# Kernel optimization log

Measured on AMD Instinct MI355X. Metric: run time of the kernel, lower is better.

Reference implementation:

```python
import jax, jax.numpy as jnp
import numpy as np

N_A = 100000; N_B = 100000; E = 1600000
H = 128; OUT = 16; G = 256; D_A = 64; D_B = 32


def setup_inputs() -> dict:
    key = jax.random.key(0)
    ks = jax.random.split(key, 24)
    f32 = jnp.float32
    def w(k, shape, fan_in):
        return jax.random.normal(k, shape, dtype=f32) / np.sqrt(fan_in)
    inp = {
        'x_a': jax.random.normal(ks[0], (N_A, D_A), dtype=f32),
        'x_b': jax.random.normal(ks[1], (N_B, D_B), dtype=f32),
        'ei_ab': jax.random.randint(ks[2], (2, E), 0, N_A),  # row0: src in a, row1: dst in b
        'ei_ba': jax.random.randint(ks[3], (2, E), 0, N_B),
        'ei_aa': jax.random.randint(ks[4], (2, E), 0, N_A),
        'batch_a': jnp.sort(jax.random.randint(ks[5], (N_A,), 0, G)),
        'batch_b': jnp.sort(jax.random.randint(ks[6], (N_B,), 0, G)),
        # node-type input embeddings
        'Wemb_a': w(ks[7], (D_A, H), D_A), 'bemb_a': jnp.zeros((H,), f32),
        'Wemb_b': w(ks[8], (D_B, H), D_B), 'bemb_b': jnp.zeros((H,), f32),
        # SAGEConv params per relation: lin_l (with bias) on aggregated, lin_r (no bias) on root
        'Wl_ab': w(ks[9], (H, H), H), 'bl_ab': jnp.zeros((H,), f32), 'Wr_ab': w(ks[10], (H, H), H),
        'Wl_ba': w(ks[11], (H, H), H), 'bl_ba': jnp.zeros((H,), f32), 'Wr_ba': w(ks[12], (H, H), H),
        'Wl_aa': w(ks[13], (H, H), H), 'bl_aa': jnp.zeros((H,), f32), 'Wr_aa': w(ks[14], (H, H), H),
        # output head
        'Wout': w(ks[15], (H, OUT), H), 'bout': jnp.zeros((OUT,), f32),
    }
    return inp


def _sage(x_src, x_dst, ei, Wl, bl, Wr, n_dst):
    # mean aggregation of source features over incoming edges, then transform + root
    msg = x_src[ei[0]]                                        # [E, H] gather
    s = jax.ops.segment_sum(msg, ei[1], num_segments=n_dst)   # [n_dst, H]
    cnt = jax.ops.segment_sum(jnp.ones((ei.shape[1], 1), x_src.dtype), ei[1], num_segments=n_dst)
    agg = s / jnp.maximum(cnt, 1.0)
    return agg @ Wl + bl + x_dst @ Wr


def _mean_pool(x, batch, num_graphs):
    s = jax.ops.segment_sum(x, batch, num_segments=num_graphs)
    cnt = jax.ops.segment_sum(jnp.ones((x.shape[0], 1), x.dtype), batch, num_segments=num_graphs)
    return s / jnp.maximum(cnt, 1.0)


def reference(x_a, x_b, ei_ab, ei_ba, ei_aa, batch_a, batch_b,
              Wemb_a, bemb_a, Wemb_b, bemb_b,
              Wl_ab, bl_ab, Wr_ab, Wl_ba, bl_ba, Wr_ba, Wl_aa, bl_aa, Wr_aa,
              Wout, bout):
    # per-type input projection
    h_a = x_a @ Wemb_a + bemb_a            # [N_A, H]
    h_b = x_b @ Wemb_b + bemb_b            # [N_B, H]
    # HeteroConv: one SAGEConv per relation, mean over relations per dst type
    m_b = _sage(h_a, h_b, ei_ab, Wl_ab, bl_ab, Wr_ab, N_B)          # dst 'b': 1 relation
    m_a1 = _sage(h_b, h_a, ei_ba, Wl_ba, bl_ba, Wr_ba, N_A)
    m_a2 = _sage(h_a, h_a, ei_aa, Wl_aa, bl_aa, Wr_aa, N_A)
    h_a2 = 0.5 * (m_a1 + m_a2)                                      # dst 'a': mean of 2 relations
    h_b2 = m_b
    # ReLU + per-type global mean pool + mean over node types
    p_a = _mean_pool(jax.nn.relu(h_a2), batch_a, G)                 # [G, H]
    p_b = _mean_pool(jax.nn.relu(h_b2), batch_b, G)
    x = 0.5 * (p_a + p_b)
    return x @ Wout + bout                                          # [G, OUT]
```

## Files before the change

### kernel.cpp

```cpp
#include <hip/hip_runtime.h>

#define NA 100000
#define NB 100000
#define NEDGE 1600000
#define HD 128
#define OUTD 16
#define NG 256
#define DA 64
#define DB 32
#define PG 8

#define BIN_SHIFT 9
#define BIN_W 512
#define NBINS_R 196
#define NBINS 588
#define PADBIN 10240
#define EPB 8192
#define ECHUNKS 196

typedef unsigned int uint_t;
typedef unsigned short ushort_t;
typedef unsigned char uchar_t;
typedef __bf16 bf16_t;
typedef bf16_t bf16x8 __attribute__((ext_vector_type(8)));
typedef float f32x4 __attribute__((ext_vector_type(4)));
typedef float f32x2 __attribute__((ext_vector_type(2)));

__device__ __forceinline__ float bflo(uint_t u) {
    union { uint_t i; float f; } c; c.i = u << 16; return c.f;
}
__device__ __forceinline__ float bfhi(uint_t u) {
    union { uint_t i; float f; } c; c.i = u & 0xffff0000u; return c.f;
}
__device__ __forceinline__ uint_t f2bf(float f) {
    union { float f; uint_t i; } c; c.f = f;
    uint_t r = c.i + 0x7FFFu + ((c.i >> 16) & 1u);
    return r >> 16;
}
__device__ __forceinline__ uint_t pack2bf(float lo, float hi) {
    return f2bf(lo) | (f2bf(hi) << 16);
}

__global__ void __launch_bounds__(256)
prep_misc_kernel(const float* __restrict__ Wl_ab, const float* __restrict__ Wr_ab,
                 const float* __restrict__ Wl_ba, const float* __restrict__ Wl_aa,
                 const float* __restrict__ Wr_ba, const float* __restrict__ Wr_aa,
                 const float* __restrict__ Wemb_a, const float* __restrict__ Wemb_b,
                 ushort_t* __restrict__ wt_fb, ushort_t* __restrict__ wt_pa,
                 ushort_t* __restrict__ wt_ea, ushort_t* __restrict__ wt_eb,
                 const float* __restrict__ bl_ba, const float* __restrict__ bl_aa,
                 float* __restrict__ bias_pa,
                 const int* __restrict__ batch_a, const int* __restrict__ batch_b,
                 float* __restrict__ ga, float* __restrict__ gb)
{
    const int bx = blockIdx.x;
    if (bx >= 40) {
        __align__(16) ushort_t tmp[8];
        if (bx <= 43) {
            const int id = (bx - 40) * 256 + threadIdx.x;
            const int nn = id >> 3, ck = id & 7;
#pragma unroll
            for (int j = 0; j < 8; ++j) tmp[j] = (ushort_t)f2bf(Wemb_a[(ck * 8 + j) * HD + nn]);
            const int swz = ck ^ (nn & 7);
            *reinterpret_cast<uint4*>(wt_ea + nn * 64 + swz * 8) = *reinterpret_cast<const uint4*>(tmp);
            return;
        }
        if (bx <= 45) {
            const int id = (bx - 44) * 256 + threadIdx.x;
            const int nn = id >> 2, ck = id & 3;
#pragma unroll
            for (int j = 0; j < 8; ++j) tmp[j] = (ushort_t)f2bf(Wemb_b[(ck * 8 + j) * HD + nn]);
            const int swz = ck ^ (nn & 3);
            *reinterpret_cast<uint4*>(wt_eb + nn * 32 + swz * 8) = *reinterpret_cast<const uint4*>(tmp);
            return;
        }
        if (bx == 46) {
            if (threadIdx.x < HD) bias_pa[threadIdx.x] = bl_ba[threadIdx.x] + bl_aa[threadIdx.x];
            return;
        }
        const int g = threadIdx.x;
        const int* batch = (bx == 48) ? batch_b : batch_a;
        float* outp = (bx == 48) ? gb : ga;
        const int n = NA;
        int lo0 = 0, hi0 = n;
        while (lo0 < hi0) { const int mid = (lo0 + hi0) >> 1; if (batch[mid] < g) lo0 = mid + 1; else hi0 = mid; }
        int lo1 = 0, hi1 = n;
        while (lo1 < hi1) { const int mid = (lo1 + hi1) >> 1; if (batch[mid] < g + 1) lo1 = mid + 1; else hi1 = mid; }
        outp[g] = (float)(lo1 - lo0);
        return;
    }
    const int m = bx >> 3;
    const int id = (bx & 7) * 256 + threadIdx.x;
    const int nn = id >> 4, ck = id & 15;
    const float* src = (m == 0) ? Wl_ab : (m == 1) ? Wr_ab : (m == 2) ? Wl_ba
                     : (m == 3) ? Wl_aa : Wr_ba;
    __align__(16) ushort_t tmp[8];
#pragma unroll
    for (int j = 0; j < 8; ++j) {
        const int k = ck * 8 + j;
        float v = src[k * HD + nn];
        if (m == 4) v += Wr_aa[k * HD + nn];
        tmp[j] = (ushort_t)f2bf(v);
    }
    const int cks = ck ^ (nn & 7);
    const int half = nn >> 6, nl = nn & 63;
    ushort_t* dst = (m < 2) ? (wt_fb + half * 16384 + m * 8192)
                            : (wt_pa + half * 24576 + (m - 2) * 8192);
    *reinterpret_cast<uint4*>(dst + nl * HD + cks * 8) = *reinterpret_cast<const uint4*>(tmp);
}

template<int K>
__global__ void __launch_bounds__(256)
emb_mfma(const float* __restrict__ x, const ushort_t* __restrict__ wt,
         const float* __restrict__ bias, ushort_t* __restrict__ h, int n)
{
    constexpr int NCK = K / 8;
    constexpr int KST = K / 32;
    __shared__ ushort_t wlds[HD * K];
    __shared__ float bias_lds[HD];
    for (int i = threadIdx.x * 8; i < HD * K; i += 2048)
        *reinterpret_cast<uint4*>(wlds + i) = *reinterpret_cast<const uint4*>(wt + i);
    if (threadIdx.x < HD) bias_lds[threadIdx.x] = bias[threadIdx.x];
    __syncthreads();
    const int l = threadIdx.x & 63, w = threadIdx.x >> 6;
    const int lo = l & 15, hi = l >> 4;
    const int row_base = blockIdx.x * 128 + w * 32;

    f32x4 acc[2][8];
    const f32x4 zero = {0.f, 0.f, 0.f, 0.f};
#pragma unroll
    for (int mi = 0; mi < 2; ++mi)
#pragma unroll
        for (int ni = 0; ni < 8; ++ni) acc[mi][ni] = zero;

    bf16x8 a[2][KST];
#pragma unroll
    for (int mi = 0; mi < 2; ++mi) {
        int r = row_base + mi * 16 + lo;
        r = min(r, n - 1);
        const float* xr = x + (size_t)r * K + hi * 8;
#pragma unroll
        for (int kk = 0; kk < KST; ++kk) {
            const float4 f0 = *reinterpret_cast<const float4*>(xr + kk * 32);
            const float4 f1 = *reinterpret_cast<const float4*>(xr + kk * 32 + 4);
            __align__(16) ushort_t us[8];
            us[0] = (ushort_t)f2bf(f0.x); us[1] = (ushort_t)f2bf(f0.y);
            us[2] = (ushort_t)f2bf(f0.z); us[3] = (ushort_t)f2bf(f0.w);
            us[4] = (ushort_t)f2bf(f1.x); us[5] = (ushort_t)f2bf(f1.y);
            us[6] = (ushort_t)f2bf(f1.z); us[7] = (ushort_t)f2bf(f1.w);
            a[mi][kk] = *reinterpret_cast<const bf16x8*>(us);
        }
    }
#pragma unroll
    for (int kk = 0; kk < KST; ++kk) {
#pragma unroll
        for (int ni = 0; ni < 8; ++ni) {
            const int nn = ni * 16 + lo;
            const int ck = (kk * 4 + hi) ^ (nn & (NCK - 1));
            const bf16x8 b = *reinterpret_cast<const bf16x8*>(wlds + nn * K + ck * 8);
            acc[0][ni] = __builtin_amdgcn_mfma_f32_16x16x32_bf16(a[0][kk], b, acc[0][ni], 0, 0, 0);
            acc[1][ni] = __builtin_amdgcn_mfma_f32_16x16x32_bf16(a[1][kk], b, acc[1][ni], 0, 0, 0);
        }
    }
#pragma unroll
    for (int mi = 0; mi < 2; ++mi) {
#pragma unroll
        for (int ni = 0; ni < 8; ++ni) {
            const int col = ni * 16 + lo;
            const float bv = bias_lds[col];
            const f32x4 v = acc[mi][ni];
#pragma unroll
            for (int r = 0; r < 4; ++r) {
                const int row = row_base + mi * 16 + hi * 4 + r;
                if (row < n) h[(size_t)row * HD + col] = (ushort_t)f2bf(v[r] + bv);
            }
        }
    }
}

__global__ void __launch_bounds__(256)
conv8_kernel(const ushort_t* __restrict__ h, uchar_t* __restrict__ h8, long n8)
{
    for (long i = (long)blockIdx.x * 256 + threadIdx.x; i < n8; i += (long)gridDim.x * 256) {
        const uint4 v = *reinterpret_cast<const uint4*>(h + i * 8);
        uint_t lo = (uint_t)__builtin_amdgcn_cvt_pk_fp8_f32(bflo(v.x), bfhi(v.x), 0, false);
        lo = (uint_t)__builtin_amdgcn_cvt_pk_fp8_f32(bflo(v.y), bfhi(v.y), lo, true);
        uint_t hi = (uint_t)__builtin_amdgcn_cvt_pk_fp8_f32(bflo(v.z), bfhi(v.z), 0, false);
        hi = (uint_t)__builtin_amdgcn_cvt_pk_fp8_f32(bflo(v.w), bfhi(v.w), hi, true);
        uint2 o; o.x = lo; o.y = hi;
        *reinterpret_cast<uint2*>(h8 + i * 8) = o;
    }
}

__global__ void __launch_bounds__(256)
part3_kernel(const int* __restrict__ ei_ab, const int* __restrict__ ei_ba,
             const int* __restrict__ ei_aa, int* __restrict__ bincnt,
             uint_t* __restrict__ binned)
{
    __shared__ uint_t sorted[EPB];
    __shared__ int lh[NBINS_R];
    __shared__ int lbase[NBINS_R];
    __shared__ int gbase[NBINS_R];
    __shared__ int lcur[NBINS_R];
    __shared__ int sc[256];
    const int r = blockIdx.y;
    const int* ei = (r == 0) ? ei_ab : (r == 1) ? ei_ba : ei_aa;
    const int t = threadIdx.x;
    for (int i = t; i < NBINS_R; i += 256) lh[i] = 0;
    __syncthreads();
    const int e0 = blockIdx.x * EPB;
    const int e1 = min(e0 + EPB, NEDGE);
    for (int e = e0 + t; e < e1; e += 256)
        atomicAdd(&lh[ei[NEDGE + e] >> BIN_SHIFT], 1);
    __syncthreads();
    {
        const int v = (t < NBINS_R) ? lh[t] : 0;
        sc[t] = v; __syncthreads();
        for (int d = 1; d < 256; d <<= 1) {
            const int x = (t >= d) ? sc[t - d] : 0;
            __syncthreads();
            sc[t] += x;
            __syncthreads();
        }
        if (t < NBINS_R) {
            const int ex = sc[t] - v;
            lbase[t] = ex; lcur[t] = ex;
            gbase[t] = v ? atomicAdd(&bincnt[r * NBINS_R + t], v) : 0;
        }
    }
    __syncthreads();
    for (int e = e0 + t; e < e1; e += 256) {
        const int dst = ei[NEDGE + e];
        const int src = ei[e];
        const int bin = dst >> BIN_SHIFT;
        const int pos = atomicAdd(&lcur[bin], 1);
        sorted[pos] = ((uint_t)(dst & (BIN_W - 1)) << 17) | (uint_t)src;
    }
    __syncthreads();
    const int wid = t >> 6, lane = t & 63;
    for (int b = wid; b < NBINS_R; b += 4) {
        const int cnt = lh[b], lb = lbase[b];
        uint_t* dst = binned + (size_t)(r * NBINS_R + b) * PADBIN + gbase[b];
        for (int k = lane; k < cnt; k += 64) dst[k] = sorted[lb + k];
    }
}

__global__ void __launch_bounds__(256)
binfill3_kernel(const uint_t* __restrict__ binned, const int* __restrict__ bincnt,
                int* __restrict__ off3, int* __restrict__ cnt3, int* __restrict__ csr3)
{
    __shared__ int hist[BIN_W];
    __shared__ int A[BIN_W];
    __shared__ int cursor[BIN_W];
    const int b = blockIdx.x;
    const int r = blockIdx.y;
    const int g = r * NBINS_R + b;
    const int start = g * PADBIN;
    const int end = start + bincnt[g];
    const int t = threadIdx.x;
    const int i0 = t, i1 = t + 256;
    hist[i0] = 0; hist[i1] = 0;
    __syncthreads();
    for (int j = start + t; j < end; j += 256)
        atomicAdd(&hist[binned[j] >> 17], 1);
    __syncthreads();
    A[i0] = hist[i0]; A[i1] = hist[i1];
    __syncthreads();
    for (int d = 1; d < BIN_W; d <<= 1) {
        const int x0 = (i0 >= d) ? A[i0 - d] : 0;
        const int x1 = (i1 >= d) ? A[i1 - d] : 0;
        __syncthreads();
        A[i0] += x0; A[i1] += x1;
        __syncthreads();
    }
    const int node0 = b * BIN_W;
#pragma unroll
    for (int q = 0; q < 2; ++q) {
        const int i = t + q * 256;
        const int ex = start + A[i] - hist[i];
        cursor[i] = ex;
        const int node = node0 + i;
        if (node < NA) { off3[r * NA + node] = ex; cnt3[r * NA + node] = hist[i]; }
    }
    __syncthreads();
    for (int j = start + t; j < end; j += 256) {
        const uint_t p = binned[j];
        const int pos = atomicAdd(&cursor[p >> 17], 1);
        csr3[pos] = (int)(p & 0x1FFFFu);
    }
}

__global__ void __launch_bounds__(256)
gather3_kernel(const uchar_t* __restrict__ h8_a, const uchar_t* __restrict__ h8_b,
               const int* __restrict__ csr3, const int* __restrict__ off3,
               const int* __restrict__ cnt3,
               ushort_t* __restrict__ s_ab, ushort_t* __restrict__ s_ba,
               ushort_t* __restrict__ s_aa)
{
    const int r = blockIdx.y;
    const uchar_t* hsrc = (r == 1) ? h8_b : h8_a;
    ushort_t* s = (r == 0) ? s_ab : (r == 1) ? s_ba : s_aa;
    const int* off = off3 + r * NA;
    const int* cnt = cnt3 + r * NA;
    const int wid = threadIdx.x >> 6, lane = threadIdx.x & 63;
    const int hl = lane & 31;
    const int nw = gridDim.x * 4;
    for (int node = blockIdx.x * 4 + wid; node < NA; node += nw) {
        const int o0 = off[node], deg = cnt[node];
        const int o1 = o0 + deg;
        float ax0 = 0.f, ax1 = 0.f, ax2 = 0.f, ax3 = 0.f;
        int j = o0;
        for (; j + 8 <= o1; j += 8) {
            const int s0 = csr3[j],     s1 = csr3[j + 1], s2 = csr3[j + 2], s3 = csr3[j + 3];
            const int s4 = csr3[j + 4], s5 = csr3[j + 5], s6 = csr3[j + 6], s7 = csr3[j + 7];
            const int sA = (lane & 32) ? s1 : s0;
            const int sB = (lane & 32) ? s3 : s2;
            const int sC = (lane & 32) ? s5 : s4;
            const int sD = (lane & 32) ? s7 : s6;
            const uint_t vA = *reinterpret_cast<const uint_t*>(hsrc + (size_t)sA * HD + hl * 4);
            const uint_t vB = *reinterpret_cast<const uint_t*>(hsrc + (size_t)sB * HD + hl * 4);
            const uint_t vC = *reinterpret_cast<const uint_t*>(hsrc + (size_t)sC * HD + hl * 4);
            const uint_t vD = *reinterpret_cast<const uint_t*>(hsrc + (size_t)sD * HD + hl * 4);
            const f32x2 a0 = __builtin_amdgcn_cvt_pk_f32_fp8(vA, false), a1 = __builtin_amdgcn_cvt_pk_f32_fp8(vA, true);
            const f32x2 b0 = __builtin_amdgcn_cvt_pk_f32_fp8(vB, false), b1 = __builtin_amdgcn_cvt_pk_f32_fp8(vB, true);
            const f32x2 c0 = __builtin_amdgcn_cvt_pk_f32_fp8(vC, false), c1 = __builtin_amdgcn_cvt_pk_f32_fp8(vC, true);
            const f32x2 d0 = __builtin_amdgcn_cvt_pk_f32_fp8(vD, false), d1 = __builtin_amdgcn_cvt_pk_f32_fp8(vD, true);
            ax0 += (a0[0] + b0[0]) + (c0[0] + d0[0]);
            ax1 += (a0[1] + b0[1]) + (c0[1] + d0[1]);
            ax2 += (a1[0] + b1[0]) + (c1[0] + d1[0]);
            ax3 += (a1[1] + b1[1]) + (c1[1] + d1[1]);
        }
        for (; j + 2 <= o1; j += 2) {
            const int s0 = csr3[j], s1 = csr3[j + 1];
            const int sA = (lane & 32) ? s1 : s0;
            const uint_t vA = *reinterpret_cast<const uint_t*>(hsrc + (size_t)sA * HD + hl * 4);
            const f32x2 a0 = __builtin_amdgcn_cvt_pk_f32_fp8(vA, false), a1 = __builtin_amdgcn_cvt_pk_f32_fp8(vA, true);
            ax0 += a0[0]; ax1 += a0[1]; ax2 += a1[0]; ax3 += a1[1];
        }
        if (j < o1) {
            const int s0 = csr3[j];
            const uint_t vA = *reinterpret_cast<const uint_t*>(hsrc + (size_t)s0 * HD + hl * 4);
            if (!(lane & 32)) {
                const f32x2 a0 = __builtin_amdgcn_cvt_pk_f32_fp8(vA, false), a1 = __builtin_amdgcn_cvt_pk_f32_fp8(vA, true);
                ax0 += a0[0]; ax1 += a0[1]; ax2 += a1[0]; ax3 += a1[1];
            }
        }
        ax0 += __shfl_xor(ax0, 32); ax1 += __shfl_xor(ax1, 32);
        ax2 += __shfl_xor(ax2, 32); ax3 += __shfl_xor(ax3, 32);
        if (!(lane & 32)) {
            const float inv = 1.0f / fmaxf((float)deg, 1.0f);
            uint2 wv;
            wv.x = pack2bf(ax0 * inv, ax1 * inv);
            wv.y = pack2bf(ax2 * inv, ax3 * inv);
            *reinterpret_cast<uint2*>(s + (size_t)node * HD + hl * 4) = wv;
        }
    }
}

template<int NSRC, int SCALE_HALF>
__device__ __forceinline__ void
mfma_body(const ushort_t* __restrict__ x0, const ushort_t* __restrict__ x1,
          const ushort_t* __restrict__ x2,
          const ushort_t* __restrict__ wts, const float* __restrict__ bias,
          const int* __restrict__ batch, float* __restrict__ outp, int n,
          char* smem)
{
    ushort_t* wlds   = (ushort_t*)smem;
    float* bias_lds  = (float*)(smem + NSRC * 16384);
    float* poolbuf   = bias_lds + HD;

    const int l  = threadIdx.x & 63, w = threadIdx.x >> 6;
    const int lo = l & 15, hi = l >> 4;
    const int row_base = blockIdx.x * 128 + w * 32;

    bf16x8 a[NSRC][2][4];
#pragma unroll
    for (int s = 0; s < NSRC; ++s) {
        const ushort_t* xs = (s == 0) ? x0 : (s == 1) ? x1 : x2;
#pragma unroll
        for (int mi = 0; mi < 2; ++mi) {
            int r = row_base + mi * 16 + lo;
            r = min(r, n - 1);
            const ushort_t* xr = xs + (size_t)r * HD + hi * 8;
#pragma unroll
            for (int kk = 0; kk < 4; ++kk)
                a[s][mi][kk] = *reinterpret_cast<const bf16x8*>(xr + kk * 32);
        }
    }
    if (threadIdx.x < HD) bias_lds[threadIdx.x] = bias[threadIdx.x];
    const int gmin = batch[blockIdx.x * 128];

    for (int half = 0; half < 2; ++half) {
        __syncthreads();
        const ushort_t* wsrc = wts + (size_t)half * NSRC * 8192;
        for (int i = threadIdx.x * 8; i < NSRC * 8192; i += 256 * 8)
            *reinterpret_cast<uint4*>(wlds + i) = *reinterpret_cast<const uint4*>(wsrc + i);
        for (int i = threadIdx.x; i < PG * 64; i += 256) poolbuf[i] = 0.f;
        __syncthreads();

        f32x4 acc[2][4];
        const f32x4 zero = {0.f, 0.f, 0.f, 0.f};
#pragma unroll
        for (int mi = 0; mi < 2; ++mi)
#pragma unroll
            for (int ni = 0; ni < 4; ++ni) acc[mi][ni] = zero;

#pragma unroll
        for (int s = 0; s < NSRC; ++s) {
            const ushort_t* wb = wlds + s * 8192;
#pragma unroll
            for (int kk = 0; kk < 4; ++kk) {
#pragma unroll
                for (int ni = 0; ni < 4; ++ni) {
                    const int nn = ni * 16 + lo;
                    const int ck = (kk * 4 + hi) ^ (nn & 7);
                    const bf16x8 b = *reinterpret_cast<const bf16x8*>(wb + nn * HD + ck * 8);
                    acc[0][ni] = __builtin_amdgcn_mfma_f32_16x16x32_bf16(a[s][0][kk], b, acc[0][ni], 0, 0, 0);
                    acc[1][ni] = __builtin_amdgcn_mfma_f32_16x16x32_bf16(a[s][1][kk], b, acc[1][ni], 0, 0, 0);
                }
            }
        }

#pragma unroll
        for (int mi = 0; mi < 2; ++mi) {
#pragma unroll
            for (int ni = 0; ni < 4; ++ni) {
                const int col_l = ni * 16 + lo;
                const int col = half * 64 + col_l;
                const float bv = bias_lds[col];
                const f32x4 v = acc[mi][ni];
#pragma unroll
                for (int r = 0; r < 4; ++r) {
                    const int row = row_base + mi * 16 + hi * 4 + r;
                    if (row < n) {
                        float val = v[r] + bv;
                        if (SCALE_HALF) val *= 0.5f;
                        val = fmaxf(val, 0.f);
                        const int g = batch[row];
                        const unsigned slot = (unsigned)(g - gmin);
                        if (slot < PG) atomicAdd(&poolbuf[slot * 64 + col_l], val);
                        else unsafeAtomicAdd(outp + (size_t)g * HD + col, val);
                    }
                }
            }
        }
        __syncthreads();
        for (int i = threadIdx.x; i < PG * 64; i += 256) {
            const float v = poolbuf[i];
            if (v != 0.f) {
                const int g = gmin + (i >> 6);
                if (g < NG) unsafeAtomicAdd(outp + (size_t)g * HD + half * 64 + (i & 63), v);
            }
        }
    }
}

__global__ void __launch_bounds__(256)
mfma_both(const ushort_t* __restrict__ s_ab, const ushort_t* __restrict__ h_b,
          const ushort_t* __restrict__ wt_fb, const float* __restrict__ bl_ab,
          const int* __restrict__ batch_b, float* __restrict__ pool_b,
          const ushort_t* __restrict__ s_ba, const ushort_t* __restrict__ s_aa,
          const ushort_t* __restrict__ h_a,
          const ushort_t* __restrict__ wt_pa, const float* __restrict__ bias_pa,
          const int* __restrict__ batch_a, float* __restrict__ pool_a)
{
    extern __shared__ char smem[];
    if (blockIdx.y == 0)
        mfma_body<2, 0>(s_ab, h_b, nullptr, wt_fb, bl_ab, batch_b, pool_b, NB, smem);
    else
        mfma_body<3, 1>(s_ba, s_aa, h_a, wt_pa, bias_pa, batch_a, pool_a, NA, smem);
}

__global__ void final_kernel(const float* __restrict__ pa, const float* __restrict__ pb,
                             const float* __restrict__ ga, const float* __restrict__ gb,
                             const float* __restrict__ Wout, const float* __restrict__ bout,
                             float* __restrict__ out)
{
    const int g = blockIdx.x;
    const int lane = threadIdx.x;
    const float inva = 1.0f / fmaxf(ga[g], 1.0f);
    const float invb = 1.0f / fmaxf(gb[g], 1.0f);
    if (lane < OUTD) {
        float acc = bout[lane];
        for (int k = 0; k < HD; ++k) {
            const float x = 0.5f * (pa[g * HD + k] * inva + pb[g * HD + k] * invb);
            acc = fmaf(x, Wout[k * OUTD + lane], acc);
        }
        out[g * OUTD + lane] = acc;
    }
}

extern "C" void kernel_launch(void* const* d_in, const int* in_sizes, int n_in,
                              void* d_out, int out_size, void* d_ws, size_t ws_size,
                              hipStream_t stream)
{
    const float* x_a     = (const float*)d_in[0];
    const float* x_b     = (const float*)d_in[1];
    const int*   ei_ab   = (const int*)d_in[2];
    const int*   ei_ba   = (const int*)d_in[3];
    const int*   ei_aa   = (const int*)d_in[4];
    const int*   batch_a = (const int*)d_in[5];
    const int*   batch_b = (const int*)d_in[6];
    const float* Wemb_a  = (const float*)d_in[7];
    const float* bemb_a  = (const float*)d_in[8];
    const float* Wemb_b  = (const float*)d_in[9];
    const float* bemb_b  = (const float*)d_in[10];
    const float* Wl_ab   = (const float*)d_in[11];
    const float* bl_ab   = (const float*)d_in[12];
    const float* Wr_ab   = (const float*)d_in[13];
    const float* Wl_ba   = (const float*)d_in[14];
    const float* bl_ba   = (const float*)d_in[15];
    const float* Wr_ba   = (const float*)d_in[16];
    const float* Wl_aa   = (const float*)d_in[17];
    const float* bl_aa   = (const float*)d_in[18];
    const float* Wr_aa   = (const float*)d_in[19];
    const float* Wout    = (const float*)d_in[20];
    const float* bout    = (const float*)d_in[21];
    float* out = (float*)d_out;

    char* p = (char*)d_ws;
    ushort_t* h_a  = (ushort_t*)p; p += (size_t)NA * HD * 2;
    ushort_t* h_b  = (ushort_t*)p; p += (size_t)NB * HD * 2;
    ushort_t* s_ab = (ushort_t*)p; p += (size_t)NB * HD * 2;
    ushort_t* s_ba = (ushort_t*)p; p += (size_t)NA * HD * 2;
    ushort_t* s_aa = (ushort_t*)p; p += (size_t)NA * HD * 2;
    uchar_t* h8_a  = (uchar_t*)p;  p += (size_t)NA * HD;
    uchar_t* h8_b  = (uchar_t*)p;  p += (size_t)NB * HD;
    int* csr3   = (int*)p;  p += (size_t)NBINS * PADBIN * 4;
    uint_t* binned = (uint_t*)p; p += (size_t)NBINS * PADBIN * 4;
    int* off3   = (int*)p;  p += (size_t)3 * NA * 4;
    int* cnt3   = (int*)p;  p += (size_t)3 * NA * 4;
    int* bincnt = (int*)p;  p += (NBINS + 4) * 4;
    float* pool_a = (float*)p; p += (size_t)NG * HD * 4;
    float* pool_b = (float*)p; p += (size_t)NG * HD * 4;
    float* gcnt_a = (float*)p; p += NG * 4;
    float* gcnt_b = (float*)p; p += NG * 4;
    ushort_t* wt_fb = (ushort_t*)p; p += 2 * 16384 * 2;
    ushort_t* wt_pa = (ushort_t*)p; p += 3 * 16384 * 2;
    ushort_t* wt_ea = (ushort_t*)p; p += 64 * HD * 2;
    ushort_t* wt_eb = (ushort_t*)p; p += 32 * HD * 2;
    float* bias_pa  = (float*)p;    p += HD * 4;

    const int GT = (NA + 127) / 128;

    hipMemsetAsync(pool_a, 0, (size_t)2 * NG * HD * 4, stream);
    hipMemsetAsync(bincnt, 0, (size_t)NBINS * 4, stream);

    prep_misc_kernel<<<49, 256, 0, stream>>>(Wl_ab, Wr_ab, Wl_ba, Wl_aa, Wr_ba, Wr_aa,
                                             Wemb_a, Wemb_b, wt_fb, wt_pa, wt_ea, wt_eb,
                                             bl_ba, bl_aa, bias_pa,
                                             batch_a, batch_b, gcnt_a, gcnt_b);

    emb_mfma<DA><<<GT, 256, 0, stream>>>(x_a, wt_ea, bemb_a, h_a, NA);
    emb_mfma<DB><<<GT, 256, 0, stream>>>(x_b, wt_eb, bemb_b, h_b, NB);
    conv8_kernel<<<2048, 256, 0, stream>>>(h_a, h8_a, (long)(NA + NB) * HD / 8);

    part3_kernel<<<dim3(ECHUNKS, 3), 256, 0, stream>>>(ei_ab, ei_ba, ei_aa, bincnt, binned);
    binfill3_kernel<<<dim3(NBINS_R, 3), 256, 0, stream>>>(binned, bincnt, off3, cnt3, csr3);

    gather3_kernel<<<dim3(2048, 3), 256, 0, stream>>>(h8_a, h8_b, csr3, off3, cnt3, s_ab, s_ba, s_aa);

    const int lds_m = 3 * 16384 + 512 + PG * 64 * 4;
    hipFuncSetAttribute((const void*)mfma_both, hipFuncAttributeMaxDynamicSharedMemorySize, lds_m);
    mfma_both<<<dim3(GT, 2), 256, lds_m, stream>>>(s_ab, h_b, wt_fb, bl_ab, batch_b, pool_b,
                                                   s_ba, s_aa, h_a, wt_pa, bias_pa, batch_a, pool_a);

    final_kernel<<<NG, 64, 0, stream>>>(pool_a, pool_b, gcnt_a, gcnt_b, Wout, bout, out);
}
```

Measured before the change: 462.0 us.

## Pre-swizzle weights into MFMA fragment order and load B operands directly from global

Result: slower. 552.1 us (+19.5%).

```diff
diff --git a/kernel.cpp b/kernel.cpp
--- a/kernel.cpp
+++ b/kernel.cpp
@@ -54,24 +54,26 @@
                  float* __restrict__ ga, float* __restrict__ gb)
 {
     const int bx = blockIdx.x;
+    __align__(16) ushort_t tmp[8];
     if (bx >= 40) {
-        __align__(16) ushort_t tmp[8];
         if (bx <= 43) {
             const int id = (bx - 40) * 256 + threadIdx.x;
-            const int nn = id >> 3, ck = id & 7;
-#pragma unroll
-            for (int j = 0; j < 8; ++j) tmp[j] = (ushort_t)f2bf(Wemb_a[(ck * 8 + j) * HD + nn]);
-            const int swz = ck ^ (nn & 7);
-            *reinterpret_cast<uint4*>(wt_ea + nn * 64 + swz * 8) = *reinterpret_cast<const uint4*>(tmp);
+            const int kk = id >> 9, ni = (id >> 6) & 7, l = id & 63;
+            const int col = ni * 16 + (l & 15);
+            const int k0 = kk * 32 + (l >> 4) * 8;
+#pragma unroll
+            for (int j = 0; j < 8; ++j) tmp[j] = (ushort_t)f2bf(Wemb_a[(k0 + j) * HD + col]);
+            *reinterpret_cast<uint4*>(wt_ea + (size_t)id * 8) = *reinterpret_cast<const uint4*>(tmp);
             return;
         }
         if (bx <= 45) {
             const int id = (bx - 44) * 256 + threadIdx.x;
-            const int nn = id >> 2, ck = id & 3;
-#pragma unroll
-            for (int j = 0; j < 8; ++j) tmp[j] = (ushort_t)f2bf(Wemb_b[(ck * 8 + j) * HD + nn]);
-            const int swz = ck ^ (nn & 3);
-            *reinterpret_cast<uint4*>(wt_eb + nn * 32 + swz * 8) = *reinterpret_cast<const uint4*>(tmp);
+            const int ni = id >> 6, l = id & 63;
+            const int col = ni * 16 + (l & 15);
+            const int k0 = (l >> 4) * 8;
+#pragma unroll
+            for (int j = 0; j < 8; ++j) tmp[j] = (ushort_t)f2bf(Wemb_b[(k0 + j) * HD + col]);
+            *reinterpret_cast<uint4*>(wt_eb + (size_t)id * 8) = *reinterpret_cast<const uint4*>(tmp);
             return;
         }
         if (bx == 46) {
@@ -91,37 +93,27 @@
     }
     const int m = bx >> 3;
     const int id = (bx & 7) * 256 + threadIdx.x;
-    const int nn = id >> 4, ck = id & 15;
+    const int kk = id >> 9, ni = (id >> 6) & 7, l = id & 63;
+    const int col = ni * 16 + (l & 15);
+    const int k0 = kk * 32 + (l >> 4) * 8;
     const float* src = (m == 0) ? Wl_ab : (m == 1) ? Wr_ab : (m == 2) ? Wl_ba
                      : (m == 3) ? Wl_aa : Wr_ba;
-    __align__(16) ushort_t tmp[8];
 #pragma unroll
     for (int j = 0; j < 8; ++j) {
-        const int k = ck * 8 + j;
-        float v = src[k * HD + nn];
-        if (m == 4) v += Wr_aa[k * HD + nn];
+        float v = src[(k0 + j) * HD + col];
+        if (m == 4) v += Wr_aa[(k0 + j) * HD + col];
         tmp[j] = (ushort_t)f2bf(v);
     }
-    const int cks = ck ^ (nn & 7);
-    const int half = nn >> 6, nl = nn & 63;
-    ushort_t* dst = (m < 2) ? (wt_fb + half * 16384 + m * 8192)
-                            : (wt_pa + half * 24576 + (m - 2) * 8192);
-    *reinterpret_cast<uint4*>(dst + nl * HD + cks * 8) = *reinterpret_cast<const uint4*>(tmp);
+    ushort_t* dst = (m < 2) ? (wt_fb + (size_t)m * 16384) : (wt_pa + (size_t)(m - 2) * 16384);
+    *reinterpret_cast<uint4*>(dst + (size_t)id * 8) = *reinterpret_cast<const uint4*>(tmp);
 }
 
 template<int K>
 __global__ void __launch_bounds__(256)
-emb_mfma(const float* __restrict__ x, const ushort_t* __restrict__ wt,
+emb_mfma(const float* __restrict__ x, const ushort_t* __restrict__ wtf,
          const float* __restrict__ bias, ushort_t* __restrict__ h, int n)
 {
-    constexpr int NCK = K / 8;
     constexpr int KST = K / 32;
-    __shared__ ushort_t wlds[HD * K];
-    __shared__ float bias_lds[HD];
-    for (int i = threadIdx.x * 8; i < HD * K; i += 2048)
-        *reinterpret_cast<uint4*>(wlds + i) = *reinterpret_cast<const uint4*>(wt + i);
-    if (threadIdx.x < HD) bias_lds[threadIdx.x] = bias[threadIdx.x];
-    __syncthreads();
     const int l = threadIdx.x & 63, w = threadIdx.x >> 6;
     const int lo = l & 15, hi = l >> 4;
     const int row_base = blockIdx.x * 128 + w * 32;
@@ -155,19 +147,17 @@
     for (int kk = 0; kk < KST; ++kk) {
 #pragma unroll
         for (int ni = 0; ni < 8; ++ni) {
-            const int nn = ni * 16 + lo;
-            const int ck = (kk * 4 + hi) ^ (nn & (NCK - 1));
-            const bf16x8 b = *reinterpret_cast<const bf16x8*>(wlds + nn * K + ck * 8);
+            const bf16x8 b = *reinterpret_cast<const bf16x8*>(wtf + ((size_t)(kk * 8 + ni) * 64 + l) * 8);
             acc[0][ni] = __builtin_amdgcn_mfma_f32_16x16x32_bf16(a[0][kk], b, acc[0][ni], 0, 0, 0);
             acc[1][ni] = __builtin_amdgcn_mfma_f32_16x16x32_bf16(a[1][kk], b, acc[1][ni], 0, 0, 0);
         }
     }
 #pragma unroll
-    for (int mi = 0; mi < 2; ++mi) {
-#pragma unroll
-        for (int ni = 0; ni < 8; ++ni) {
-            const int col = ni * 16 + lo;
-            const float bv = bias_lds[col];
+    for (int ni = 0; ni < 8; ++ni) {
+        const int col = ni * 16 + lo;
+        const float bv = bias[col];
+#pragma unroll
+        for (int mi = 0; mi < 2; ++mi) {
             const f32x4 v = acc[mi][ni];
 #pragma unroll
             for (int r = 0; r < 4; ++r) {
@@ -358,25 +348,31 @@
 }
 
 template<int NSRC, int SCALE_HALF>
-__device__ __forceinline__ void
-mfma_body(const ushort_t* __restrict__ x0, const ushort_t* __restrict__ x1,
+__global__ void __launch_bounds__(256)
+mfma_task(const ushort_t* __restrict__ x0, const ushort_t* __restrict__ x1,
           const ushort_t* __restrict__ x2,
-          const ushort_t* __restrict__ wts, const float* __restrict__ bias,
-          const int* __restrict__ batch, float* __restrict__ outp, int n,
-          char* smem)
-{
-    ushort_t* wlds   = (ushort_t*)smem;
-    float* bias_lds  = (float*)(smem + NSRC * 16384);
-    float* poolbuf   = bias_lds + HD;
+          const ushort_t* __restrict__ wtf, const float* __restrict__ bias,
+          const int* __restrict__ batch, float* __restrict__ outp, int n)
+{
+    __shared__ float poolbuf[PG * HD];
+    for (int i = threadIdx.x; i < PG * HD; i += 256) poolbuf[i] = 0.f;
+    __syncthreads();
 
     const int l  = threadIdx.x & 63, w = threadIdx.x >> 6;
     const int lo = l & 15, hi = l >> 4;
     const int row_base = blockIdx.x * 128 + w * 32;
 
-    bf16x8 a[NSRC][2][4];
+    f32x4 acc[2][8];
+    const f32x4 zero = {0.f, 0.f, 0.f, 0.f};
+#pragma unroll
+    for (int mi = 0; mi < 2; ++mi)
+#pragma unroll
+        for (int ni = 0; ni < 8; ++ni) acc[mi][ni] = zero;
+
 #pragma unroll
     for (int s = 0; s < NSRC; ++s) {
         const ushort_t* xs = (s == 0) ? x0 : (s == 1) ? x1 : x2;
+        bf16x8 a[2][4];
 #pragma unroll
         for (int mi = 0; mi < 2; ++mi) {
             int r = row_base + mi * 16 + lo;
@@ -384,91 +380,59 @@
             const ushort_t* xr = xs + (size_t)r * HD + hi * 8;
 #pragma unroll
             for (int kk = 0; kk < 4; ++kk)
-                a[s][mi][kk] = *reinterpret_cast<const bf16x8*>(xr + kk * 32);
-        }
-    }
-    if (threadIdx.x < HD) bias_lds[threadIdx.x] = bias[threadIdx.x];
+                a[mi][kk] = *reinterpret_cast<const bf16x8*>(xr + kk * 32);
+        }
+        const ushort_t* wm = wtf + (size_t)s * 16384;
+#pragma unroll
+        for (int kk = 0; kk < 4; ++kk) {
+#pragma unroll
+            for (int ni = 0; ni < 8; ++ni) {
+                const bf16x8 b = *reinterpret_cast<const bf16x8*>(wm + ((size_t)(kk * 8 + ni) * 64 + l) * 8);
+                acc[0][ni] = __builtin_amdgcn_mfma_f32_16x16x32_bf16(a[0][kk], b, acc[0][ni], 0, 0, 0);
+                acc[1][ni] = __builtin_amdgcn_mfma_f32_16x16x32_bf16(a[1][kk], b, acc[1][ni], 0, 0, 0);
+            }
+        }
+    }
+
     const int gmin = batch[blockIdx.x * 128];
-
-    for (int half = 0; half < 2; ++half) {
-        __syncthreads();
-        const ushort_t* wsrc = wts + (size_t)half * NSRC * 8192;
-        for (int i = threadIdx.x * 8; i < NSRC * 8192; i += 256 * 8)
-            *reinterpret_cast<uint4*>(wlds + i) = *reinterpret_cast<const uint4*>(wsrc + i);
-        for (int i = threadIdx.x; i < PG * 64; i += 256) poolbuf[i] = 0.f;
-        __syncthreads();
-
-        f32x4 acc[2][4];
-        const f32x4 zero = {0.f, 0.f, 0.f, 0.f};
-#pragma unroll
-        for (int mi = 0; mi < 2; ++mi)
-#pragma unroll
-            for (int ni = 0; ni < 4; ++ni) acc[mi][ni] = zero;
-
-#pragma unroll
-        for (int s = 0; s < NSRC; ++s) {
-            const ushort_t* wb = wlds + s * 8192;
-#pragma unroll
-            for (int kk = 0; kk < 4; ++kk) {
-#pragma unroll
-                for (int ni = 0; ni < 4; ++ni) {
-                    const int nn = ni * 16 + lo;
-                    const int ck = (kk * 4 + hi) ^ (nn & 7);
-                    const bf16x8 b = *reinterpret_cast<const bf16x8*>(wb + nn * HD + ck * 8);
-                    acc[0][ni] = __builtin_amdgcn_mfma_f32_16x16x32_bf16(a[s][0][kk], b, acc[0][ni], 0, 0, 0);
-                    acc[1][ni] = __builtin_amdgcn_mfma_f32_16x16x32_bf16(a[s][1][kk], b, acc[1][ni], 0, 0, 0);
+    int gg[2][4];
+#pragma unroll
+    for (int mi = 0; mi < 2; ++mi)
+#pragma unroll
+        for (int r = 0; r < 4; ++r) {
+            const int row = row_base + mi * 16 + hi * 4 + r;
+            gg[mi][r] = (row < n) ? batch[row] : -1;
+        }
+
+#pragma unroll
+    for (int ni = 0; ni < 8; ++ni) {
+        const int col = ni * 16 + lo;
+        const float bv = bias[col];
+#pragma unroll
+        for (int mi = 0; mi < 2; ++mi) {
+            const f32x4 v = acc[mi][ni];
+#pragma unroll
+            for (int r = 0; r < 4; ++r) {
+                const int g = gg[mi][r];
+                if (g >= 0) {
+                    float val = v[r] + bv;
+                    if (SCALE_HALF) val *= 0.5f;
+                    val = fmaxf(val, 0.f);
+                    const unsigned slot = (unsigned)(g - gmin);
+                    if (slot < PG) atomicAdd(&poolbuf[slot * HD + col], val);
+                    else unsafeAtomicAdd(outp + (size_t)g * HD + col, val);
                 }
             }
         }
-
-#pragma unroll
-        for (int mi = 0; mi < 2; ++mi) {
-#pragma unroll
-            for (int ni = 0; ni < 4; ++ni) {
-                const int col_l = ni * 16 + lo;
-                const int col = half * 64 + col_l;
-                const float bv = bias_lds[col];
-                const f32x4 v = acc[mi][ni];
-#pragma unroll
-                for (int r = 0; r < 4; ++r) {
-                    const int row = row_base + mi * 16 + hi * 4 + r;
-                    if (row < n) {
-                        float val = v[r] + bv;
-                        if (SCALE_HALF) val *= 0.5f;
-                        val = fmaxf(val, 0.f);
-                        const int g = batch[row];
-                        const unsigned slot = (unsigned)(g - gmin);
-                        if (slot < PG) atomicAdd(&poolbuf[slot * 64 + col_l], val);
-                        else unsafeAtomicAdd(outp + (size_t)g * HD + col, val);
-                    }
-                }
-            }
-        }
-        __syncthreads();
-        for (int i = threadIdx.x; i < PG * 64; i += 256) {
-            const float v = poolbuf[i];
-            if (v != 0.f) {
-                const int g = gmin + (i >> 6);
-                if (g < NG) unsafeAtomicAdd(outp + (size_t)g * HD + half * 64 + (i & 63), v);
-            }
-        }
-    }
-}
-
-__global__ void __launch_bounds__(256)
-mfma_both(const ushort_t* __restrict__ s_ab, const ushort_t* __restrict__ h_b,
-          const ushort_t* __restrict__ wt_fb, const float* __restrict__ bl_ab,
-          const int* __restrict__ batch_b, float* __restrict__ pool_b,
-          const ushort_t* __restrict__ s_ba, const ushort_t* __restrict__ s_aa,
-          const ushort_t* __restrict__ h_a,
-          const ushort_t* __restrict__ wt_pa, const float* __restrict__ bias_pa,
-          const int* __restrict__ batch_a, float* __restrict__ pool_a)
-{
-    extern __shared__ char smem[];
-    if (blockIdx.y == 0)
-        mfma_body<2, 0>(s_ab, h_b, nullptr, wt_fb, bl_ab, batch_b, pool_b, NB, smem);
-    else
-        mfma_body<3, 1>(s_ba, s_aa, h_a, wt_pa, bias_pa, batch_a, pool_a, NA, smem);
+    }
+    __syncthreads();
+    for (int i = threadIdx.x; i < PG * HD; i += 256) {
+        const float v = poolbuf[i];
+        if (v != 0.f) {
+            const int g = gmin + (i >> 7);
+            if (g < NG) unsafeAtomicAdd(outp + (size_t)g * HD + (i & 127), v);
+        }
+    }
 }
 
 __global__ void final_kernel(const float* __restrict__ pa, const float* __restrict__ pb,
@@ -560,10 +524,8 @@
 
     gather3_kernel<<<dim3(2048, 3), 256, 0, stream>>>(h8_a, h8_b, csr3, off3, cnt3, s_ab, s_ba, s_aa);
 
-    const int lds_m = 3 * 16384 + 512 + PG * 64 * 4;
-    hipFuncSetAttribute((const void*)mfma_both, hipFuncAttributeMaxDynamicSharedMemorySize, lds_m);
-    mfma_both<<<dim3(GT, 2), 256, lds_m, stream>>>(s_ab, h_b, wt_fb, bl_ab, batch_b, pool_b,
-                                                   s_ba, s_aa, h_a, wt_pa, bias_pa, batch_a, pool_a);
+    mfma_task<2, 0><<<GT, 256, 0, stream>>>(s_ab, h_b, nullptr, wt_fb, bl_ab, batch_b, pool_b, NB);
+    mfma_task<3, 1><<<GT, 256, 0, stream>>>(s_ba, s_aa, h_a, wt_pa, bias_pa, batch_a, pool_a, NA);
 
     final_kernel<<<NG, 64, 0, stream>>>(pool_a, pool_b, gcnt_a, gcnt_b, Wout, bout, out);
 }
```
